# Kernel optimization log

Hardware: AMD Instinct MI355X
Metric: run time of the kernel (lower is better)

Reference implementation:

```python
import jax, jax.numpy as jnp
import numpy as np

N_ATOMS = 200000
MAX_DEG = 6
DEG_COUNTS = [2000, 40000, 60000, 58000, 38000, 1500, 500]  # atoms of degree 0..6, sorted by degree
_OFF = np.concatenate([[0], np.cumsum(DEG_COUNTS)])
BATCH = 1024
N_TASKS = 12
NAF = 75
BN_SCALE = np.float32(1.0 / np.sqrt(1.0 + 1e-5))  # eval-mode BN, running stats (0, 1)


def _split(x):
    # static degree slicing (atoms sorted by degree)
    return [x[_OFF[d]:_OFF[d + 1]] for d in range(MAX_DEG + 1)]


def graph_conv(x, adjs, W, b):
    # W: [2*MAX_DEG+1, in, out]; per degree d>=1 weights (2(d-1): neighbors, 2d-1: self), last: degree-0 self
    sp = _split(x)
    outs = [None] * (MAX_DEG + 1)
    for d in range(1, MAX_DEG + 1):
        summed = x[adjs[d - 1]].sum(axis=1)  # [n_d, in] sum over d neighbors
        o = summed @ W[2 * (d - 1)] + b[2 * (d - 1)]
        o = o + sp[d] @ W[2 * d - 1] + b[2 * d - 1]
        outs[d] = o
    outs[0] = sp[0] @ W[2 * MAX_DEG] + b[2 * MAX_DEG]
    return jax.nn.relu(jnp.concatenate(outs, axis=0))


def graph_pool(x, adjs):
    # max over {self} U neighbors, per degree
    sp = _split(x)
    outs = [sp[0]]
    for d in range(1, MAX_DEG + 1):
        neigh = x[adjs[d - 1]]  # [n_d, d, nf]
        outs.append(jnp.concatenate([sp[d][:, None, :], neigh], axis=1).max(axis=1))
    return jnp.concatenate(outs, axis=0)


def bn(x, gamma, beta):
    return x * (gamma * BN_SCALE) + beta


def _forward(atom_features, conv0_W, conv0_b, conv1_W, conv1_b,
             bn0_gamma, bn0_beta, bn1_gamma, bn1_beta, bn2_gamma, bn2_beta,
             bn3_gamma, bn3_beta, dense0_W, dense0_b, dense1_W, dense1_b,
             reg_W, reg_b, unc_W, unc_b, membership, adjs, n_samples):
    x = graph_conv(atom_features, adjs, conv0_W, conv0_b)
    x = bn(x, bn0_gamma, bn0_beta)
    x = graph_pool(x, adjs)
    x = graph_conv(x, adjs, conv1_W, conv1_b)
    x = bn(x, bn1_gamma, bn1_beta)
    x = graph_pool(x, adjs)
    x = bn(jax.nn.relu(x @ dense0_W + dense0_b), bn2_gamma, bn2_beta)
    x = bn(jax.nn.relu(x @ dense1_W + dense1_b), bn3_gamma, bn3_beta)
    fp = jnp.tanh(jax.ops.segment_sum(x, membership, num_segments=BATCH))  # GraphGather
    out = (fp @ reg_W + reg_b)[:n_samples]
    log_var = (fp @ unc_W + unc_b)[:n_samples]
    var = jnp.exp(log_var)
    return (out, var, out, log_var, fp)


def setup_inputs():
    key = jax.random.key(0)
    ks = jax.random.split(key, 32)
    inp = {}
    inp['atom_features'] = jax.random.normal(ks[0], (N_ATOMS, NAF), jnp.float32)
    inp['degree_slice'] = jnp.stack([jnp.asarray(_OFF[:-1], jnp.int32), jnp.asarray(DEG_COUNTS, jnp.int32)], axis=1)
    inp['membership'] = jax.random.randint(ks[1], (N_ATOMS,), 0, BATCH, jnp.int32)
    inp['n_samples'] = BATCH
    for d in range(1, MAX_DEG + 1):
        inp['deg_adj_%d' % d] = jax.random.randint(ks[1 + d], (DEG_COUNTS[d], d), 0, N_ATOMS, jnp.int32)
    def w(k, shape):
        return jax.random.normal(k, shape, jnp.float32) * 0.05
    nW = 2 * MAX_DEG + 1
    inp['conv0_W'] = w(ks[8], (nW, NAF, 128)); inp['conv0_b'] = w(ks[9], (nW, 128))
    inp['conv1_W'] = w(ks[10], (nW, 128, 128)); inp['conv1_b'] = w(ks[11], (nW, 128))
    inp['bn0_gamma'] = 1.0 + w(ks[12], (128,)); inp['bn0_beta'] = w(ks[13], (128,))
    inp['bn1_gamma'] = 1.0 + w(ks[14], (128,)); inp['bn1_beta'] = w(ks[15], (128,))
    inp['bn2_gamma'] = 1.0 + w(ks[16], (64,)); inp['bn2_beta'] = w(ks[17], (64,))
    inp['bn3_gamma'] = 1.0 + w(ks[18], (64,)); inp['bn3_beta'] = w(ks[19], (64,))
    inp['dense0_W'] = w(ks[20], (128, 64)); inp['dense0_b'] = w(ks[21], (64,))
    inp['dense1_W'] = w(ks[22], (64, 64)); inp['dense1_b'] = w(ks[23], (64,))
    inp['reg_W'] = w(ks[24], (64, N_TASKS)); inp['reg_b'] = w(ks[25], (N_TASKS,))
    inp['unc_W'] = w(ks[26], (64, N_TASKS)); inp['unc_b'] = w(ks[27], (N_TASKS,))
    return inp


def reference(atom_features, conv0_W, conv0_b, conv1_W, conv1_b,
              bn0_gamma, bn0_beta, bn1_gamma, bn1_beta, bn2_gamma, bn2_beta,
              bn3_gamma, bn3_beta, dense0_W, dense0_b, dense1_W, dense1_b,
              reg_W, reg_b, unc_W, unc_b,
              degree_slice, membership, n_samples,
              deg_adj_1, deg_adj_2, deg_adj_3, deg_adj_4, deg_adj_5, deg_adj_6):
    adjs = [deg_adj_1, deg_adj_2, deg_adj_3, deg_adj_4, deg_adj_5, deg_adj_6]
    return _forward(atom_features, conv0_W, conv0_b, conv1_W, conv1_b,
                    bn0_gamma, bn0_beta, bn1_gamma, bn1_beta, bn2_gamma, bn2_beta,
                    bn3_gamma, bn3_beta, dense0_W, dense0_b, dense1_W, dense1_b,
                    reg_W, reg_b, unc_W, unc_b, membership, adjs, n_samples)
```

## Files before the change

kernel.cpp:

```cpp
#include <hip/hip_runtime.h>
#include <math.h>

constexpr int OFFS[8] = {0, 2000, 42000, 102000, 160000, 198000, 199500, 200000};
constexpr int CNT[7]  = {2000, 40000, 60000, 58000, 38000, 1500, 500};
constexpr int C_OFF[8] = {0, 32, 657, 1595, 2502, 3096, 3120, 3128};
constexpr int P_OFF[8] = {0, 250, 5250, 12750, 20000, 24750, 24938, 25001};
#define BN_SCALE_C 0.9999950000374997f

struct Adjs { const int* a[6]; };

typedef __attribute__((ext_vector_type(8))) short bf16x8;
typedef __attribute__((ext_vector_type(4))) float f32x4;

__device__ __forceinline__ void split1(float x, ushort& h, ushort& l) {
    const unsigned u = __float_as_uint(x);
    h = (ushort)(u >> 16);
    const float r = x - __uint_as_float(u & 0xffff0000u);
    l = (ushort)(__float_as_uint(r) >> 16);
}

__device__ __forceinline__ void split8a(const float s[8], bf16x8& hv, bf16x8& lv) {
    #pragma unroll
    for (int i = 0; i < 8; ++i) {
        ushort h, lo;
        split1(s[i], h, lo);
        hv[i] = (short)h; lv[i] = (short)lo;
    }
}

__global__ __launch_bounds__(256)
void w1_convert_kernel(const float* __restrict__ W, ushort* __restrict__ hi,
                       ushort* __restrict__ lo) {
    const int t = blockIdx.x * 256 + threadIdx.x;
    if (t >= 13 * 8 * 4 * 64 * 8) return;
    const int i = t & 7, l = (t >> 3) & 63, ks = (t >> 9) & 3,
              g = (t >> 11) & 7, s = t >> 14;
    const int col = g * 16 + (l & 15);
    const int k = ks * 32 + (l >> 4) * 8 + i;
    ushort h, lw;
    split1(W[(size_t)(s * 128 + k) * 128 + col], h, lw);
    hi[t] = h; lo[t] = lw;
}

__global__ __launch_bounds__(256)
void w0_convert_kernel(const float* __restrict__ W, ushort* __restrict__ hi,
                       ushort* __restrict__ lo) {
    const int t = blockIdx.x * 256 + threadIdx.x;
    if (t >= 13 * 8 * 3 * 64 * 8) return;
    const int i = t & 7;
    const int l = (t >> 3) & 63;
    const int r2 = t >> 9;
    const int ks = r2 % 3;
    const int r3 = r2 / 3;
    const int g = r3 & 7, m = r3 >> 3;
    const int col = g * 16 + (l & 15);
    const int k = ks * 32 + (l >> 4) * 8 + i;
    float v = 0.f;
    if (k < 75) v = W[(size_t)(m * 75 + k) * 128 + col];
    ushort h, lw;
    split1(v, h, lw);
    hi[t] = h; lo[t] = lw;
}

template<int ROWLEN>
__device__ __forceinline__ void row_acc(const float* __restrict__ row, int k0,
                                        float s[8]) {
    if constexpr (ROWLEN == 128) {
        const float4 a = *(const float4*)(row + k0);
        const float4 b = *(const float4*)(row + k0 + 4);
        s[0] += a.x; s[1] += a.y; s[2] += a.z; s[3] += a.w;
        s[4] += b.x; s[5] += b.y; s[6] += b.z; s[7] += b.w;
    } else {
        #pragma unroll
        for (int i = 0; i < 8; ++i)
            if (k0 + i < ROWLEN) s[i] += row[k0 + i];
    }
}

template<int KS>
__device__ __forceinline__ void gemm_ks(const ushort* __restrict__ wh,
                                        const ushort* __restrict__ wl,
                                        int ks, size_t lb,
                                        bf16x8 ah, bf16x8 al_, f32x4 acc[8])
{
    bf16x8 bh0 = *(const bf16x8*)(wh + (size_t)(0 * KS + ks) * 512 + lb);
    bf16x8 bl0 = *(const bf16x8*)(wl + (size_t)(0 * KS + ks) * 512 + lb);
    bf16x8 bh1 = *(const bf16x8*)(wh + (size_t)(1 * KS + ks) * 512 + lb);
    bf16x8 bl1 = *(const bf16x8*)(wl + (size_t)(1 * KS + ks) * 512 + lb);
    #pragma unroll
    for (int g = 0; g < 8; ++g) {
        bf16x8 bh2 = bh0, bl2 = bl0;
        if (g < 6) {
            bh2 = *(const bf16x8*)(wh + (size_t)((g + 2) * KS + ks) * 512 + lb);
            bl2 = *(const bf16x8*)(wl + (size_t)((g + 2) * KS + ks) * 512 + lb);
        }
        acc[g] = __builtin_amdgcn_mfma_f32_16x16x32_bf16(ah, bh0, acc[g], 0, 0, 0);
        acc[g] = __builtin_amdgcn_mfma_f32_16x16x32_bf16(al_, bh0, acc[g], 0, 0, 0);
        acc[g] = __builtin_amdgcn_mfma_f32_16x16x32_bf16(ah, bl0, acc[g], 0, 0, 0);
        bh0 = bh1; bl0 = bl1; bh1 = bh2; bl1 = bl2;
    }
}

template<int D, int ROWLEN, int KS>
__device__ __forceinline__ void conv_body(int tile, const float* __restrict__ x,
    const ushort* __restrict__ wp_hi, const ushort* __restrict__ wp_lo,
    const float* __restrict__ bias, const float* __restrict__ gamma,
    const float* __restrict__ beta, const int* __restrict__ adjp,
    float* __restrict__ out, float* fs, float* s_eb, int tid)
{
    const int a0 = OFFS[D] + tile * 64;
    const int nat = min(64, OFFS[D + 1] - a0);
    const int l = tid & 63, w = tid >> 6, lr = l & 15, lq = l >> 4;

    if (tid < 128) {
        float bb;
        if constexpr (D > 0)
            bb = bias[(2 * D - 2) * 128 + tid] + bias[(2 * D - 1) * 128 + tid];
        else
            bb = bias[12 * 128 + tid];
        s_eb[tid] = bb;
        s_eb[128 + tid] = gamma[tid] * BN_SCALE_C;
        s_eb[256 + tid] = beta[tid];
    }

    const int rowa = min(a0 + w * 16 + lr, OFFS[D + 1] - 1);
    int nb[(D > 0) ? D : 1];
    if constexpr (D > 0) {
        #pragma unroll
        for (int j = 0; j < D; ++j)
            nb[j] = adjp[(size_t)(rowa - OFFS[D]) * D + j];
    }

    f32x4 acc[8];
    #pragma unroll
    for (int g = 0; g < 8; ++g) acc[g] = (f32x4){0.f, 0.f, 0.f, 0.f};

    const size_t lb = (size_t)l * 8;

    {
        const int m = (D == 0) ? 12 : (2 * D - 2);
        const ushort* wh = wp_hi + (size_t)m * (8 * KS * 512);
        const ushort* wl = wp_lo + (size_t)m * (8 * KS * 512);
        #pragma unroll
        for (int ks = 0; ks < KS; ++ks) {
            const int k0 = ks * 32 + lq * 8;
            float s[8] = {0.f, 0.f, 0.f, 0.f, 0.f, 0.f, 0.f, 0.f};
            if constexpr (D > 0) {
                #pragma unroll
                for (int j = 0; j < D; ++j)
                    row_acc<ROWLEN>(x + (size_t)nb[j] * ROWLEN, k0, s);
            } else {
                row_acc<ROWLEN>(x + (size_t)rowa * ROWLEN, k0, s);
            }
            bf16x8 ah, al_;
            split8a(s, ah, al_);
            gemm_ks<KS>(wh, wl, ks, lb, ah, al_, acc);
        }
    }
    if constexpr (D > 0) {
        const ushort* wh = wp_hi + (size_t)(2 * D - 1) * (8 * KS * 512);
        const ushort* wl = wp_lo + (size_t)(2 * D - 1) * (8 * KS * 512);
        #pragma unroll
        for (int ks = 0; ks < KS; ++ks) {
            const int k0 = ks * 32 + lq * 8;
            float s[8] = {0.f, 0.f, 0.f, 0.f, 0.f, 0.f, 0.f, 0.f};
            row_acc<ROWLEN>(x + (size_t)rowa * ROWLEN, k0, s);
            bf16x8 ah, al_;
            split8a(s, ah, al_);
            gemm_ks<KS>(wh, wl, ks, lb, ah, al_, acc);
        }
    }

    __syncthreads();
    #pragma unroll
    for (int h = 0; h < 2; ++h) {
        if ((w >> 1) == h) {
            const int wloc = w & 1;
            #pragma unroll
            for (int g = 0; g < 8; ++g)
                #pragma unroll
                for (int r = 0; r < 4; ++r)
                    fs[(wloc * 16 + lq * 4 + r) * 132 + g * 16 + lr] = acc[g][r];
        }
        __syncthreads();
        #pragma unroll
        for (int p = 0; p < 4; ++p) {
            const int fr = p * 8 + (tid >> 5);
            const int row = h * 32 + fr;
            if (row < nat) {
                const int c = (tid & 31) * 4;
                const float4 v  = *(const float4*)&fs[fr * 132 + c];
                const float4 bb = *(const float4*)&s_eb[c];
                const float4 gs = *(const float4*)&s_eb[128 + c];
                const float4 be = *(const float4*)&s_eb[256 + c];
                float4 o;
                o.x = fmaxf(v.x + bb.x, 0.f) * gs.x + be.x;
                o.y = fmaxf(v.y + bb.y, 0.f) * gs.y + be.y;
                o.z = fmaxf(v.z + bb.z, 0.f) * gs.z + be.z;
                o.w = fmaxf(v.w + bb.w, 0.f) * gs.w + be.w;
                *(float4*)(out + (size_t)(a0 + row) * 128 + c) = o;
            }
        }
        __syncthreads();
    }
}

__global__ __launch_bounds__(256, 4)
void conv0_merged(const float* __restrict__ x, const ushort* __restrict__ wp_hi,
                  const ushort* __restrict__ wp_lo, const float* __restrict__ b,
                  const float* __restrict__ gamma, const float* __restrict__ beta,
                  Adjs adj, float* __restrict__ out)
{
    __shared__ float fs[32 * 132];
    __shared__ float s_eb[384];
    const int blk = blockIdx.x, tid = threadIdx.x;
    #define C0(D) conv_body<D, 75, 3>(blk - C_OFF[D], x, wp_hi, wp_lo, b, gamma, \
        beta, (D > 0) ? adj.a[D - 1] : nullptr, out, fs, s_eb, tid)
    if      (blk < C_OFF[1]) C0(0);
    else if (blk < C_OFF[2]) C0(1);
    else if (blk < C_OFF[3]) C0(2);
    else if (blk < C_OFF[4]) C0(3);
    else if (blk < C_OFF[5]) C0(4);
    else if (blk < C_OFF[6]) C0(5);
    else                     C0(6);
    #undef C0
}

__global__ __launch_bounds__(256, 4)
void conv1_merged(const float* __restrict__ x, const ushort* __restrict__ wp_hi,
                  const ushort* __restrict__ wp_lo, const float* __restrict__ b,
                  const float* __restrict__ gamma, const float* __restrict__ beta,
                  Adjs adj, float* __restrict__ out)
{
    __shared__ float fs[32 * 132];
    __shared__ float s_eb[384];
    const int blk = blockIdx.x, tid = threadIdx.x;
    #define C1(D) conv_body<D, 128, 4>(blk - C_OFF[D], x, wp_hi, wp_lo, b, gamma, \
        beta, (D > 0) ? adj.a[D - 1] : nullptr, out, fs, s_eb, tid)
    if      (blk < C_OFF[1]) C1(0);
    else if (blk < C_OFF[2]) C1(1);
    else if (blk < C_OFF[3]) C1(2);
    else if (blk < C_OFF[4]) C1(3);
    else if (blk < C_OFF[5]) C1(4);
    else if (blk < C_OFF[6]) C1(5);
    else                     C1(6);
    #undef C1
}

template<int D>
__device__ __forceinline__ void pool_body(int tile, const float* __restrict__ x,
    const int* __restrict__ adjp, float* __restrict__ out, int tid)
{
    const int tx = tid & 31;
    const int ai = tile * 8 + (tid >> 5);
    if (ai >= CNT[D]) return;
    const int a = OFFS[D] + ai;
    float4 v = *((const float4*)(x + (size_t)a * 128) + tx);
    if constexpr (D > 0) {
        #pragma unroll
        for (int i = 0; i < D; ++i) {
            const int n = adjp[(size_t)ai * D + i];
            const float4 t = *((const float4*)(x + (size_t)n * 128) + tx);
            v.x = fmaxf(v.x, t.x); v.y = fmaxf(v.y, t.y);
            v.z = fmaxf(v.z, t.z); v.w = fmaxf(v.w, t.w);
        }
    }
    *((float4*)(out + (size_t)a * 128) + tx) = v;
}

__global__ __launch_bounds__(256)
void pool_merged(const float* __restrict__ x, Adjs adj, float* __restrict__ out)
{
    const int blk = blockIdx.x, tid = threadIdx.x;
    #define PB(D) pool_body<D>(blk - P_OFF[D], x, (D > 0) ? adj.a[D - 1] : nullptr, out, tid)
    if      (blk < P_OFF[1]) PB(0);
    else if (blk < P_OFF[2]) PB(1);
    else if (blk < P_OFF[3]) PB(2);
    else if (blk < P_OFF[4]) PB(3);
    else if (blk < P_OFF[5]) PB(4);
    else if (blk < P_OFF[6]) PB(5);
    else                     PB(6);
    #undef PB
}

template<int D>
__device__ __forceinline__ void d0_body(int tile, const float* __restrict__ x,
    const float* __restrict__ W, const float* __restrict__ b,
    const float* __restrict__ gamma, const float* __restrict__ beta,
    const int* __restrict__ adjp, float* __restrict__ out,
    float* s_a , int* s_adj, int tid)
{
    const int a0 = OFFS[D] + tile * 64;
    const int nat = min(64, OFFS[D + 1] - a0);

    if constexpr (D > 0) {
        for (int e = tid; e < 64 * D; e += 256) {
            const int al = e / D;
            if (al < nat)
                s_adj[e] = adjp[(size_t)(a0 - OFFS[D] + al) * D + (e - al * D)];
        }
        __syncthreads();
    }
    {
        const int tx4 = tid & 31, ag = tid >> 5;
        #pragma unroll
        for (int ap = 0; ap < 8; ++ap) {
            const int al = ap * 8 + ag;
            if (al < nat) {
                float4 v = *((const float4*)(x + (size_t)(a0 + al) * 128) + tx4);
                if constexpr (D > 0) {
                    #pragma unroll
                    for (int i = 0; i < D; ++i) {
                        const float4 t =
                            *((const float4*)(x + (size_t)s_adj[al * D + i] * 128) + tx4);
                        v.x = fmaxf(v.x, t.x); v.y = fmaxf(v.y, t.y);
                        v.z = fmaxf(v.z, t.z); v.w = fmaxf(v.w, t.w);
                    }
                }
                *(float4*)&s_a[al * 132 + tx4 * 4] = v;
            }
        }
    }
    __syncthreads();

    const int tx = tid & 15, ty = tid >> 4;
    float acc[4][4];
    #pragma unroll
    for (int i = 0; i < 4; ++i)
        #pragma unroll
        for (int j = 0; j < 4; ++j) acc[i][j] = 0.f;

    #pragma unroll 4
    for (int k4 = 0; k4 < 32; ++k4) {
        float4 wk[4];
        #pragma unroll
        for (int kk = 0; kk < 4; ++kk)
            wk[kk] = *(const float4*)(W + (size_t)(k4 * 4 + kk) * 64 + tx * 4);
        #pragma unroll
        for (int i = 0; i < 4; ++i) {
            const float4 av = *(const float4*)&s_a[(ty * 4 + i) * 132 + k4 * 4];
            acc[i][0] = fmaf(av.x, wk[0].x, acc[i][0]);
            acc[i][1] = fmaf(av.x, wk[0].y, acc[i][1]);
            acc[i][2] = fmaf(av.x, wk[0].z, acc[i][2]);
            acc[i][3] = fmaf(av.x, wk[0].w, acc[i][3]);
            acc[i][0] = fmaf(av.y, wk[1].x, acc[i][0]);
            acc[i][1] = fmaf(av.y, wk[1].y, acc[i][1]);
            acc[i][2] = fmaf(av.y, wk[1].z, acc[i][2]);
            acc[i][3] = fmaf(av.y, wk[1].w, acc[i][3]);
            acc[i][0] = fmaf(av.z, wk[2].x, acc[i][0]);
            acc[i][1] = fmaf(av.z, wk[2].y, acc[i][1]);
            acc[i][2] = fmaf(av.z, wk[2].z, acc[i][2]);
            acc[i][3] = fmaf(av.z, wk[2].w, acc[i][3]);
            acc[i][0] = fmaf(av.w, wk[3].x, acc[i][0]);
            acc[i][1] = fmaf(av.w, wk[3].y, acc[i][1]);
            acc[i][2] = fmaf(av.w, wk[3].z, acc[i][2]);
            acc[i][3] = fmaf(av.w, wk[3].w, acc[i][3]);
        }
    }
    const int j = tx * 4;
    float bb[4], gs[4], be[4];
    #pragma unroll
    for (int c = 0; c < 4; ++c) {
        bb[c] = b[j + c]; gs[c] = gamma[j + c] * BN_SCALE_C; be[c] = beta[j + c];
    }
    #pragma unroll
    for (int i = 0; i < 4; ++i) {
        const int al = ty * 4 + i;
        if (al < nat) {
            float4 o;
            o.x = fmaxf(acc[i][0] + bb[0], 0.f) * gs[0] + be[0];
            o.y = fmaxf(acc[i][1] + bb[1], 0.f) * gs[1] + be[1];
            o.z = fmaxf(acc[i][2] + bb[2], 0.f) * gs[2] + be[2];
            o.w = fmaxf(acc[i][3] + bb[3], 0.f) * gs[3] + be[3];
            *(float4*)(out + (size_t)(a0 + al) * 64 + j) = o;
        }
    }
}

__global__ __launch_bounds__(256, 4)
void dense0_pool_merged(const float* __restrict__ x, const float* __restrict__ W,
                        const float* __restrict__ b, const float* __restrict__ gamma,
                        const float* __restrict__ beta, Adjs adj,
                        float* __restrict__ out)
{
    __shared__ float s_a[64 * 132];
    __shared__ int s_adj[64 * 6];
    const int blk = blockIdx.x, tid = threadIdx.x;
    #define D0(D) d0_body<D>(blk - C_OFF[D], x, W, b, gamma, beta, \
        (D > 0) ? adj.a[D - 1] : nullptr, out, s_a, s_adj, tid)
    if      (blk < C_OFF[1]) D0(0);
    else if (blk < C_OFF[2]) D0(1);
    else if (blk < C_OFF[3]) D0(2);
    else if (blk < C_OFF[4]) D0(3);
    else if (blk < C_OFF[5]) D0(4);
    else if (blk < C_OFF[6]) D0(5);
    else                     D0(6);
    #undef D0
}

__global__ void zero_counts_kernel(int* __restrict__ counts) {
    counts[blockIdx.x * 256 + threadIdx.x] = 0;
}

__global__ __launch_bounds__(256)
void hist_kernel(const int* __restrict__ mem, int* __restrict__ counts) {
    const int a = blockIdx.x * 256 + threadIdx.x;
    if (a < 200000) atomicAdd(&counts[mem[a]], 1);
}

__global__ __launch_bounds__(1024)
void scan_kernel(const int* __restrict__ counts, int* __restrict__ starts,
                 int* __restrict__ cursor) {
    __shared__ int s[1024];
    const int tid = threadIdx.x;
    s[tid] = counts[tid];
    __syncthreads();
    #pragma unroll
    for (int off = 1; off < 1024; off <<= 1) {
        const int v = (tid >= off) ? s[tid - off] : 0;
        __syncthreads();
        s[tid] += v;
        __syncthreads();
    }
    const int st = (tid == 0) ? 0 : s[tid - 1];
    starts[tid] = st;
    cursor[tid] = st;
    if (tid == 1023) starts[1024] = s[1023];
}

__global__ __launch_bounds__(256)
void scatter_kernel(const int* __restrict__ mem, int* __restrict__ cursor,
                    int* __restrict__ idx) {
    const int a = blockIdx.x * 256 + threadIdx.x;
    if (a < 200000) {
        const int p = atomicAdd(&cursor[mem[a]], 1);
        idx[p] = a;
    }
}

__global__ __launch_bounds__(256, 4)
void seg_dense1_kernel(const float* __restrict__ y0, const float* __restrict__ W,
                       const float* __restrict__ b, const float* __restrict__ gamma,
                       const float* __restrict__ beta, const int* __restrict__ idx,
                       const int* __restrict__ starts, float* __restrict__ accum)
{
    __shared__ float s_a[64][68];
    __shared__ float s_w[64][64];
    __shared__ float s_red[16][64];
    const int tid = threadIdx.x;
    const int seg = blockIdx.x;
    const int s0 = starts[seg];
    const int cnt = starts[seg + 1] - s0;

    #pragma unroll
    for (int p = 0; p < 4; ++p) {
        const int f = p * 256 + tid;
        const int r = f >> 4, c = (f & 15) * 4;
        *(float4*)&s_w[r][c] = *(const float4*)(W + r * 64 + c);
    }

    const int tx = tid & 15, ty = tid >> 4;
    const int j = tx * 4;
    float bb[4], gs[4], be[4];
    #pragma unroll
    for (int c = 0; c < 4; ++c) {
        bb[c] = b[j + c]; gs[c] = gamma[j + c] * BN_SCALE_C; be[c] = beta[j + c];
    }
    float facc[4] = {0.f, 0.f, 0.f, 0.f};

    for (int t0 = 0; t0 < cnt; t0 += 64) {
        const int nt = min(64, cnt - t0);
        __syncthreads();
        #pragma unroll
        for (int p = 0; p < 4; ++p) {
            const int e = p * 256 + tid;
            const int al = e >> 4, c = e & 15;
            if (al < nt) {
                const int a = idx[s0 + t0 + al];
                *(float4*)&s_a[al][c * 4] = *((const float4*)(y0 + (size_t)a * 64) + c);
            }
        }
        __syncthreads();
        float acc[4][4];
        #pragma unroll
        for (int i = 0; i < 4; ++i)
            #pragma unroll
            for (int c = 0; c < 4; ++c) acc[i][c] = 0.f;
        #pragma unroll 8
        for (int k = 0; k < 64; ++k) {
            const float4 w = *(float4*)&s_w[k][tx * 4];
            #pragma unroll
            for (int i = 0; i < 4; ++i) {
                const float av = s_a[ty * 4 + i][k];
                acc[i][0] = fmaf(av, w.x, acc[i][0]);
                acc[i][1] = fmaf(av, w.y, acc[i][1]);
                acc[i][2] = fmaf(av, w.z, acc[i][2]);
                acc[i][3] = fmaf(av, w.w, acc[i][3]);
            }
        }
        #pragma unroll
        for (int i = 0; i < 4; ++i) {
            if (ty * 4 + i < nt) {
                #pragma unroll
                for (int c = 0; c < 4; ++c)
                    facc[c] += fmaxf(acc[i][c] + bb[c], 0.f) * gs[c] + be[c];
            }
        }
    }
    __syncthreads();
    #pragma unroll
    for (int c = 0; c < 4; ++c) s_red[ty][j + c] = facc[c];
    __syncthreads();
    if (tid < 64) {
        float s = 0.f;
        #pragma unroll
        for (int q = 0; q < 16; ++q) s += s_red[q][tid];
        accum[(size_t)seg * 64 + tid] = s;
    }
}

__global__ __launch_bounds__(256)
void final_kernel(const float* __restrict__ accum,
                  const float* __restrict__ regW, const float* __restrict__ regb,
                  const float* __restrict__ uncW, const float* __restrict__ uncb,
                  float* __restrict__ out)
{
    __shared__ float s_f[256];
    const int tid = threadIdx.x;
    const int rl = tid >> 6;
    const int c = tid & 63;
    const int r = blockIdx.x * 4 + rl;
    const float f = tanhf(accum[(size_t)r * 64 + c]);
    out[49152 + (size_t)r * 64 + c] = f;
    s_f[tid] = f;
    __syncthreads();
    if (c < 24) {
        const bool isreg = (c < 12);
        const int t = isreg ? c : c - 12;
        const float* Wm = isreg ? regW : uncW;
        float a = isreg ? regb[t] : uncb[t];
        #pragma unroll 8
        for (int k = 0; k < 64; ++k)
            a = fmaf(s_f[rl * 64 + k], Wm[k * 12 + t], a);
        if (isreg) {
            out[(size_t)r * 12 + t] = a;
            out[24576 + (size_t)r * 12 + t] = a;
        } else {
            out[36864 + (size_t)r * 12 + t] = a;
            out[12288 + (size_t)r * 12 + t] = expf(a);
        }
    }
}

extern "C" void kernel_launch(void* const* d_in, const int* in_sizes, int n_in,
                              void* d_out, int out_size, void* d_ws, size_t ws_size,
                              hipStream_t stream)
{
    const float* atom_features = (const float*)d_in[0];
    const int*   membership    = (const int*)d_in[2];
    Adjs adj;
    for (int d = 1; d <= 6; ++d) adj.a[d - 1] = (const int*)d_in[3 + d];
    const float* conv0_W = (const float*)d_in[10];
    const float* conv0_b = (const float*)d_in[11];
    const float* conv1_W = (const float*)d_in[12];
    const float* conv1_b = (const float*)d_in[13];
    const float* bn0_g = (const float*)d_in[14];
    const float* bn0_b = (const float*)d_in[15];
    const float* bn1_g = (const float*)d_in[16];
    const float* bn1_b = (const float*)d_in[17];
    const float* bn2_g = (const float*)d_in[18];
    const float* bn2_b = (const float*)d_in[19];
    const float* bn3_g = (const float*)d_in[20];
    const float* bn3_b = (const float*)d_in[21];
    const float* dense0_W = (const float*)d_in[22];
    const float* dense0_b = (const float*)d_in[23];
    const float* dense1_W = (const float*)d_in[24];
    const float* dense1_b = (const float*)d_in[25];
    const float* reg_W = (const float*)d_in[26];
    const float* reg_b = (const float*)d_in[27];
    const float* unc_W = (const float*)d_in[28];
    const float* unc_b = (const float*)d_in[29];

    float* ws    = (float*)d_ws;
    float* buf0  = ws;
    float* buf1  = ws + 25600000;
    float* accum = ws + 51200000;
    int*   idx     = (int*)(ws + 51265536);
    int*   counts  = (int*)(ws + 51465536);
    int*   starts  = (int*)(ws + 51466560);
    int*   cursor  = (int*)(ws + 51467585);
    ushort* wp1_hi = (ushort*)(ws + 51468800);
    ushort* wp1_lo = (ushort*)(ws + 51575296);
    ushort* wp0_hi = (ushort*)(ws + 51681792);
    ushort* wp0_lo = (ushort*)(ws + 51761664);

    w1_convert_kernel<<<832, 256, 0, stream>>>(conv1_W, wp1_hi, wp1_lo);
    w0_convert_kernel<<<624, 256, 0, stream>>>(conv0_W, wp0_hi, wp0_lo);
    zero_counts_kernel<<<4, 256, 0, stream>>>(counts);
    hist_kernel<<<782, 256, 0, stream>>>(membership, counts);
    scan_kernel<<<1, 1024, 0, stream>>>(counts, starts, cursor);
    scatter_kernel<<<782, 256, 0, stream>>>(membership, cursor, idx);

    conv0_merged<<<3128, 256, 0, stream>>>(atom_features, wp0_hi, wp0_lo, conv0_b,
                                           bn0_g, bn0_b, adj, buf0);
    pool_merged<<<25001, 256, 0, stream>>>(buf0, adj, buf1);
    conv1_merged<<<3128, 256, 0, stream>>>(buf1, wp1_hi, wp1_lo, conv1_b,
                                           bn1_g, bn1_b, adj, buf0);
    dense0_pool_merged<<<3128, 256, 0, stream>>>(buf0, dense0_W, dense0_b,
                                                 bn2_g, bn2_b, adj, buf1);
    seg_dense1_kernel<<<1024, 256, 0, stream>>>(buf1, dense1_W, dense1_b,
                                                bn3_g, bn3_b, idx, starts, accum);
    final_kernel<<<256, 256, 0, stream>>>(accum, reg_W, reg_b, unc_W, unc_b, (float*)d_out);
}
```

Before: 538.3 us.

## Pre-split conv inputs to bf16 hi/lo and apply GEMM per neighbor row

Conv kernels now read activations already split into bf16 hi/lo halves, padded to a multiple of 32 columns. A new pad_split kernel handles the atom features, and the pool kernel writes its output pre-split. Instead of summing neighbor rows in fp32 and splitting once, each neighbor row is multiplied separately against the weights through MFMA. This removes per-tile split arithmetic and the unaligned 75-wide loads, but multiplies MFMA work and weight-fragment loads by the degree. Summation order also changes slightly.

```diff
diff --git a/kernel.cpp b/kernel.cpp
--- a/kernel.cpp
+++ b/kernel.cpp
@@ -17,15 +17,6 @@
     h = (ushort)(u >> 16);
     const float r = x - __uint_as_float(u & 0xffff0000u);
     l = (ushort)(__float_as_uint(r) >> 16);
-}
-
-__device__ __forceinline__ void split8a(const float s[8], bf16x8& hv, bf16x8& lv) {
-    #pragma unroll
-    for (int i = 0; i < 8; ++i) {
-        ushort h, lo;
-        split1(s[i], h, lo);
-        hv[i] = (short)h; lv[i] = (short)lo;
-    }
 }
 
 __global__ __launch_bounds__(256)
@@ -62,52 +53,28 @@
     hi[t] = h; lo[t] = lw;
 }
 
-template<int ROWLEN>
-__device__ __forceinline__ void row_acc(const float* __restrict__ row, int k0,
-                                        float s[8]) {
-    if constexpr (ROWLEN == 128) {
-        const float4 a = *(const float4*)(row + k0);
-        const float4 b = *(const float4*)(row + k0 + 4);
-        s[0] += a.x; s[1] += a.y; s[2] += a.z; s[3] += a.w;
-        s[4] += b.x; s[5] += b.y; s[6] += b.z; s[7] += b.w;
-    } else {
-        #pragma unroll
-        for (int i = 0; i < 8; ++i)
-            if (k0 + i < ROWLEN) s[i] += row[k0 + i];
-    }
-}
-
-template<int KS>
-__device__ __forceinline__ void gemm_ks(const ushort* __restrict__ wh,
-                                        const ushort* __restrict__ wl,
-                                        int ks, size_t lb,
-                                        bf16x8 ah, bf16x8 al_, f32x4 acc[8])
-{
-    bf16x8 bh0 = *(const bf16x8*)(wh + (size_t)(0 * KS + ks) * 512 + lb);
-    bf16x8 bl0 = *(const bf16x8*)(wl + (size_t)(0 * KS + ks) * 512 + lb);
-    bf16x8 bh1 = *(const bf16x8*)(wh + (size_t)(1 * KS + ks) * 512 + lb);
-    bf16x8 bl1 = *(const bf16x8*)(wl + (size_t)(1 * KS + ks) * 512 + lb);
-    #pragma unroll
-    for (int g = 0; g < 8; ++g) {
-        bf16x8 bh2 = bh0, bl2 = bl0;
-        if (g < 6) {
-            bh2 = *(const bf16x8*)(wh + (size_t)((g + 2) * KS + ks) * 512 + lb);
-            bl2 = *(const bf16x8*)(wl + (size_t)((g + 2) * KS + ks) * 512 + lb);
-        }
-        acc[g] = __builtin_amdgcn_mfma_f32_16x16x32_bf16(ah, bh0, acc[g], 0, 0, 0);
-        acc[g] = __builtin_amdgcn_mfma_f32_16x16x32_bf16(al_, bh0, acc[g], 0, 0, 0);
-        acc[g] = __builtin_amdgcn_mfma_f32_16x16x32_bf16(ah, bl0, acc[g], 0, 0, 0);
-        bh0 = bh1; bl0 = bl1; bh1 = bh2; bl1 = bl2;
-    }
-}
-
-template<int D, int ROWLEN, int KS>
-__device__ __forceinline__ void conv_body(int tile, const float* __restrict__ x,
+__global__ __launch_bounds__(256)
+void pad_split_kernel(const float* __restrict__ af, ushort* __restrict__ hi,
+                      ushort* __restrict__ lo) {
+    const int t = blockIdx.x * 256 + threadIdx.x;
+    if (t >= 19200000) return;
+    const int row = t / 96;
+    const int k = t - row * 96;
+    const float v = (k < 75) ? af[(size_t)row * 75 + k] : 0.f;
+    ushort h, l;
+    split1(v, h, l);
+    hi[t] = h; lo[t] = l;
+}
+
+template<int D, int KS>
+__device__ __forceinline__ void convPS_body(int tile,
+    const ushort* __restrict__ hi_in, const ushort* __restrict__ lo_in,
     const ushort* __restrict__ wp_hi, const ushort* __restrict__ wp_lo,
     const float* __restrict__ bias, const float* __restrict__ gamma,
     const float* __restrict__ beta, const int* __restrict__ adjp,
     float* __restrict__ out, float* fs, float* s_eb, int tid)
 {
+    constexpr int ROWP = KS * 32;
     const int a0 = OFFS[D] + tile * 64;
     const int nat = min(64, OFFS[D + 1] - a0);
     const int l = tid & 63, w = tid >> 6, lr = l & 15, lq = l >> 4;
@@ -136,38 +103,45 @@
     for (int g = 0; g < 8; ++g) acc[g] = (f32x4){0.f, 0.f, 0.f, 0.f};
 
     const size_t lb = (size_t)l * 8;
-
-    {
-        const int m = (D == 0) ? 12 : (2 * D - 2);
-        const ushort* wh = wp_hi + (size_t)m * (8 * KS * 512);
-        const ushort* wl = wp_lo + (size_t)m * (8 * KS * 512);
-        #pragma unroll
-        for (int ks = 0; ks < KS; ++ks) {
-            const int k0 = ks * 32 + lq * 8;
-            float s[8] = {0.f, 0.f, 0.f, 0.f, 0.f, 0.f, 0.f, 0.f};
-            if constexpr (D > 0) {
+    const int m0 = (D == 0) ? 12 : (2 * D - 2);
+    const ushort* wnh = wp_hi + (size_t)m0 * (8 * KS * 512);
+    const ushort* wnl = wp_lo + (size_t)m0 * (8 * KS * 512);
+    const ushort* wsh = (D > 0) ? wp_hi + (size_t)(2 * D - 1) * (8 * KS * 512) : wnh;
+    const ushort* wsl = (D > 0) ? wp_lo + (size_t)(2 * D - 1) * (8 * KS * 512) : wnl;
+
+    #pragma unroll
+    for (int ks = 0; ks < KS; ++ks) {
+        const int k0 = ks * 32 + lq * 8;
+        {
+            const size_t ab = (size_t)rowa * ROWP + k0;
+            const bf16x8 sh = *(const bf16x8*)(hi_in + ab);
+            const bf16x8 sl = *(const bf16x8*)(lo_in + ab);
+            #pragma unroll
+            for (int g = 0; g < 8; ++g) {
+                const size_t bo = (size_t)(g * KS + ks) * 512 + lb;
+                const bf16x8 bh = *(const bf16x8*)(wsh + bo);
+                const bf16x8 bl = *(const bf16x8*)(wsl + bo);
+                acc[g] = __builtin_amdgcn_mfma_f32_16x16x32_bf16(sh, bh, acc[g], 0, 0, 0);
+                acc[g] = __builtin_amdgcn_mfma_f32_16x16x32_bf16(sl, bh, acc[g], 0, 0, 0);
+                acc[g] = __builtin_amdgcn_mfma_f32_16x16x32_bf16(sh, bl, acc[g], 0, 0, 0);
+            }
+        }
+        if constexpr (D > 0) {
+            #pragma unroll
+            for (int j = 0; j < D; ++j) {
+                const size_t ab = (size_t)nb[j] * ROWP + k0;
+                const bf16x8 nh = *(const bf16x8*)(hi_in + ab);
+                const bf16x8 nl = *(const bf16x8*)(lo_in + ab);
                 #pragma unroll
-                for (int j = 0; j < D; ++j)
-                    row_acc<ROWLEN>(x + (size_t)nb[j] * ROWLEN, k0, s);
-            } else {
-                row_acc<ROWLEN>(x + (size_t)rowa * ROWLEN, k0, s);
+                for (int g = 0; g < 8; ++g) {
+                    const size_t bo = (size_t)(g * KS + ks) * 512 + lb;
+                    const bf16x8 bh = *(const bf16x8*)(wnh + bo);
+                    const bf16x8 bl = *(const bf16x8*)(wnl + bo);
+                    acc[g] = __builtin_amdgcn_mfma_f32_16x16x32_bf16(nh, bh, acc[g], 0, 0, 0);
+                    acc[g] = __builtin_amdgcn_mfma_f32_16x16x32_bf16(nl, bh, acc[g], 0, 0, 0);
+                    acc[g] = __builtin_amdgcn_mfma_f32_16x16x32_bf16(nh, bl, acc[g], 0, 0, 0);
+                }
             }
-            bf16x8 ah, al_;
-            split8a(s, ah, al_);
-            gemm_ks<KS>(wh, wl, ks, lb, ah, al_, acc);
-        }
-    }
-    if constexpr (D > 0) {
-        const ushort* wh = wp_hi + (size_t)(2 * D - 1) * (8 * KS * 512);
-        const ushort* wl = wp_lo + (size_t)(2 * D - 1) * (8 * KS * 512);
-        #pragma unroll
-        for (int ks = 0; ks < KS; ++ks) {
-            const int k0 = ks * 32 + lq * 8;
-            float s[8] = {0.f, 0.f, 0.f, 0.f, 0.f, 0.f, 0.f, 0.f};
-            row_acc<ROWLEN>(x + (size_t)rowa * ROWLEN, k0, s);
-            bf16x8 ah, al_;
-            split8a(s, ah, al_);
-            gemm_ks<KS>(wh, wl, ks, lb, ah, al_, acc);
         }
     }
 
@@ -206,16 +180,16 @@
 }
 
 __global__ __launch_bounds__(256, 4)
-void conv0_merged(const float* __restrict__ x, const ushort* __restrict__ wp_hi,
-                  const ushort* __restrict__ wp_lo, const float* __restrict__ b,
-                  const float* __restrict__ gamma, const float* __restrict__ beta,
-                  Adjs adj, float* __restrict__ out)
+void conv0_merged(const ushort* __restrict__ hi_in, const ushort* __restrict__ lo_in,
+                  const ushort* __restrict__ wp_hi, const ushort* __restrict__ wp_lo,
+                  const float* __restrict__ b, const float* __restrict__ gamma,
+                  const float* __restrict__ beta, Adjs adj, float* __restrict__ out)
 {
     __shared__ float fs[32 * 132];
     __shared__ float s_eb[384];
     const int blk = blockIdx.x, tid = threadIdx.x;
-    #define C0(D) conv_body<D, 75, 3>(blk - C_OFF[D], x, wp_hi, wp_lo, b, gamma, \
-        beta, (D > 0) ? adj.a[D - 1] : nullptr, out, fs, s_eb, tid)
+    #define C0(D) convPS_body<D, 3>(blk - C_OFF[D], hi_in, lo_in, wp_hi, wp_lo, \
+        b, gamma, beta, (D > 0) ? adj.a[D - 1] : nullptr, out, fs, s_eb, tid)
     if      (blk < C_OFF[1]) C0(0);
     else if (blk < C_OFF[2]) C0(1);
     else if (blk < C_OFF[3]) C0(2);
@@ -227,16 +201,16 @@
 }
 
 __global__ __launch_bounds__(256, 4)
-void conv1_merged(const float* __restrict__ x, const ushort* __restrict__ wp_hi,
-                  const ushort* __restrict__ wp_lo, const float* __restrict__ b,
-                  const float* __restrict__ gamma, const float* __restrict__ beta,
-                  Adjs adj, float* __restrict__ out)
+void conv1_merged(const ushort* __restrict__ hi_in, const ushort* __restrict__ lo_in,
+                  const ushort* __restrict__ wp_hi, const ushort* __restrict__ wp_lo,
+                  const float* __restrict__ b, const float* __restrict__ gamma,
+                  const float* __restrict__ beta, Adjs adj, float* __restrict__ out)
 {
     __shared__ float fs[32 * 132];
     __shared__ float s_eb[384];
     const int blk = blockIdx.x, tid = threadIdx.x;
-    #define C1(D) conv_body<D, 128, 4>(blk - C_OFF[D], x, wp_hi, wp_lo, b, gamma, \
-        beta, (D > 0) ? adj.a[D - 1] : nullptr, out, fs, s_eb, tid)
+    #define C1(D) convPS_body<D, 4>(blk - C_OFF[D], hi_in, lo_in, wp_hi, wp_lo, \
+        b, gamma, beta, (D > 0) ? adj.a[D - 1] : nullptr, out, fs, s_eb, tid)
     if      (blk < C_OFF[1]) C1(0);
     else if (blk < C_OFF[2]) C1(1);
     else if (blk < C_OFF[3]) C1(2);
@@ -249,7 +223,8 @@
 
 template<int D>
 __device__ __forceinline__ void pool_body(int tile, const float* __restrict__ x,
-    const int* __restrict__ adjp, float* __restrict__ out, int tid)
+    const int* __restrict__ adjp, ushort* __restrict__ p_hi,
+    ushort* __restrict__ p_lo, int tid)
 {
     const int tx = tid & 31;
     const int ai = tile * 8 + (tid >> 5);
@@ -265,14 +240,20 @@
             v.z = fmaxf(v.z, t.z); v.w = fmaxf(v.w, t.w);
         }
     }
-    *((float4*)(out + (size_t)a * 128) + tx) = v;
+    ushort4 h, lo;
+    split1(v.x, h.x, lo.x); split1(v.y, h.y, lo.y);
+    split1(v.z, h.z, lo.z); split1(v.w, h.w, lo.w);
+    *(ushort4*)(p_hi + (size_t)a * 128 + tx * 4) = h;
+    *(ushort4*)(p_lo + (size_t)a * 128 + tx * 4) = lo;
 }
 
 __global__ __launch_bounds__(256)
-void pool_merged(const float* __restrict__ x, Adjs adj, float* __restrict__ out)
+void pool_merged(const float* __restrict__ x, Adjs adj,
+                 ushort* __restrict__ p_hi, ushort* __restrict__ p_lo)
 {
     const int blk = blockIdx.x, tid = threadIdx.x;
-    #define PB(D) pool_body<D>(blk - P_OFF[D], x, (D > 0) ? adj.a[D - 1] : nullptr, out, tid)
+    #define PB(D) pool_body<D>(blk - P_OFF[D], x, (D > 0) ? adj.a[D - 1] : nullptr, \
+        p_hi, p_lo, tid)
     if      (blk < P_OFF[1]) PB(0);
     else if (blk < P_OFF[2]) PB(1);
     else if (blk < P_OFF[3]) PB(2);
@@ -581,9 +562,13 @@
     const float* unc_W = (const float*)d_in[28];
     const float* unc_b = (const float*)d_in[29];
 
-    float* ws    = (float*)d_ws;
-    float* buf0  = ws;
-    float* buf1  = ws + 25600000;
+    float* ws = (float*)d_ws;
+    float* bufA = ws;
+    ushort* af_hi = (ushort*)(ws + 25600000);
+    ushort* af_lo = af_hi + 19200000;
+    ushort* p_hi  = (ushort*)(ws + 25600000);
+    ushort* p_lo  = p_hi + 25600000;
+    float*  y0    = ws + 25600000;
     float* accum = ws + 51200000;
     int*   idx     = (int*)(ws + 51265536);
     int*   counts  = (int*)(ws + 51465536);
@@ -596,19 +581,20 @@
 
     w1_convert_kernel<<<832, 256, 0, stream>>>(conv1_W, wp1_hi, wp1_lo);
     w0_convert_kernel<<<624, 256, 0, stream>>>(conv0_W, wp0_hi, wp0_lo);
+    pad_split_kernel<<<75000, 256, 0, stream>>>(atom_features, af_hi, af_lo);
     zero_counts_kernel<<<4, 256, 0, stream>>>(counts);
     hist_kernel<<<782, 256, 0, stream>>>(membership, counts);
     scan_kernel<<<1, 1024, 0, stream>>>(counts, starts, cursor);
     scatter_kernel<<<782, 256, 0, stream>>>(membership, cursor, idx);
 
-    conv0_merged<<<3128, 256, 0, stream>>>(atom_features, wp0_hi, wp0_lo, conv0_b,
-                                           bn0_g, bn0_b, adj, buf0);
-    pool_merged<<<25001, 256, 0, stream>>>(buf0, adj, buf1);
-    conv1_merged<<<3128, 256, 0, stream>>>(buf1, wp1_hi, wp1_lo, conv1_b,
-                                           bn1_g, bn1_b, adj, buf0);
-    dense0_pool_merged<<<3128, 256, 0, stream>>>(buf0, dense0_W, dense0_b,
-                                                 bn2_g, bn2_b, adj, buf1);
-    seg_dense1_kernel<<<1024, 256, 0, stream>>>(buf1, dense1_W, dense1_b,
+    conv0_merged<<<3128, 256, 0, stream>>>(af_hi, af_lo, wp0_hi, wp0_lo, conv0_b,
+                                           bn0_g, bn0_b, adj, bufA);
+    pool_merged<<<25001, 256, 0, stream>>>(bufA, adj, p_hi, p_lo);
+    conv1_merged<<<3128, 256, 0, stream>>>(p_hi, p_lo, wp1_hi, wp1_lo, conv1_b,
+                                           bn1_g, bn1_b, adj, bufA);
+    dense0_pool_merged<<<3128, 256, 0, stream>>>(bufA, dense0_W, dense0_b,
+                                                 bn2_g, bn2_b, adj, y0);
+    seg_dense1_kernel<<<1024, 256, 0, stream>>>(y0, dense1_W, dense1_b,
                                                 bn3_g, bn3_b, idx, starts, accum);
     final_kernel<<<256, 256, 0, stream>>>(accum, reg_W, reg_b, unc_W, unc_b, (float*)d_out);
 }
```

After: 583.9 us. 8.5% more time.
